# Optimization experiments

Hardware: AMD Instinct MI355X
Metric: run time of the kernel (lower is better)

The kernel has to match this reference:

```python
import jax, jax.numpy as jnp
import numpy as np

EPS = 1e-08

def setup_inputs() -> dict:
    key = jax.random.key(0)
    k1, k2 = jax.random.split(key)
    h = jax.random.normal(k1, (4, 4096, 2048), dtype=jnp.float32)
    vectors = jax.random.normal(k2, (16, 2048), dtype=jnp.float32) * 0.01
    return {"h": h, "vectors": vectors}

def reference(h, vectors):
    # Chain of k Householder reflections applied sequentially (loop-carried h).
    def step(h, v):
        v_norm_sq = jnp.maximum(jnp.dot(v, v), EPS)
        proj = jnp.einsum('bsd,d->bs', h, v)  # [B,S]
        h = h - (2.0 / v_norm_sq) * proj[..., None] * v
        return h, None
    h, _ = jax.lax.scan(step, h, vectors)
    return h
```

## Files before the change

kernel.cpp:

```cpp
#include <hip/hip_runtime.h>

#define HH_EPS 1e-8f

constexpr int D      = 2048;
constexpr int K      = 16;
constexpr int R      = 4;
constexpr int CHUNKS = D / (64 * 4);
constexpr int NROWS  = 4 * 4096;

__global__ void __launch_bounds__(64) hh_norms_kernel(const float* __restrict__ vecs,
                                                      float* __restrict__ c) {
    int k = blockIdx.x;
    int lane = threadIdx.x;
    const float4* v4 = (const float4*)(vecs + k * D);
    float s = 0.f;
#pragma unroll
    for (int j = 0; j < CHUNKS; ++j) {
        float4 v = v4[j * 64 + lane];
        s += v.x * v.x + v.y * v.y + v.z * v.z + v.w * v.w;
    }
#pragma unroll
    for (int off = 32; off >= 1; off >>= 1)
        s += __shfl_xor(s, off);
    if (lane == 0) c[k] = 2.0f / fmaxf(s, HH_EPS);
}

__device__ __forceinline__ void hh_phase(float4 (&h)[R][CHUNKS],
                                         float4 (&vcur)[CHUNKS],
                                         float4 (&vnext)[CHUNKS],
                                         const float4* __restrict__ v4base,
                                         const float* __restrict__ c,
                                         int k, int lane) {
    const float4* vn = v4base + ((k + 1) & 15) * (D / 4);
#pragma unroll
    for (int j = 0; j < CHUNKS; ++j)
        vnext[j] = vn[j * 64 + lane];

    float ck = c[k];

    float dot[R];
#pragma unroll
    for (int r = 0; r < R; ++r) dot[r] = 0.f;
#pragma unroll
    for (int j = 0; j < CHUNKS; ++j) {
#pragma unroll
        for (int r = 0; r < R; ++r) {
            dot[r] += h[r][j].x * vcur[j].x + h[r][j].y * vcur[j].y
                    + h[r][j].z * vcur[j].z + h[r][j].w * vcur[j].w;
        }
    }

#pragma unroll
    for (int off = 32; off >= 1; off >>= 1) {
#pragma unroll
        for (int r = 0; r < R; ++r)
            dot[r] += __shfl_xor(dot[r], off);
    }

    float t[R];
#pragma unroll
    for (int r = 0; r < R; ++r) t[r] = ck * dot[r];

#pragma unroll
    for (int j = 0; j < CHUNKS; ++j) {
#pragma unroll
        for (int r = 0; r < R; ++r) {
            h[r][j].x -= t[r] * vcur[j].x;
            h[r][j].y -= t[r] * vcur[j].y;
            h[r][j].z -= t[r] * vcur[j].z;
            h[r][j].w -= t[r] * vcur[j].w;
        }
    }
}

__global__ void __launch_bounds__(256, 2) hh_apply_kernel(const float* __restrict__ h_in,
                                                          const float* __restrict__ vecs,
                                                          const float* __restrict__ c,
                                                          float* __restrict__ h_out) {
    int wave = (int)((blockIdx.x * blockDim.x + threadIdx.x) >> 6);
    int lane = threadIdx.x & 63;
    int base_row = wave * R;

    float4 h[R][CHUNKS];
#pragma unroll
    for (int r = 0; r < R; ++r) {
        const float4* row = (const float4*)(h_in + (size_t)(base_row + r) * D);
#pragma unroll
        for (int j = 0; j < CHUNKS; ++j)
            h[r][j] = row[j * 64 + lane];
    }

    const float4* v4base = (const float4*)vecs;

    float4 va[CHUNKS], vb[CHUNKS];
#pragma unroll
    for (int j = 0; j < CHUNKS; ++j)
        va[j] = v4base[j * 64 + lane];

#pragma unroll 1
    for (int k = 0; k < K; k += 2) {
        hh_phase(h, va, vb, v4base, c, k, lane);
        hh_phase(h, vb, va, v4base, c, k + 1, lane);
    }

#pragma unroll
    for (int r = 0; r < R; ++r) {
        float4* row = (float4*)(h_out + (size_t)(base_row + r) * D);
#pragma unroll
        for (int j = 0; j < CHUNKS; ++j)
            row[j * 64 + lane] = h[r][j];
    }
}

extern "C" void kernel_launch(void* const* d_in, const int* in_sizes, int n_in,
                              void* d_out, int out_size, void* d_ws, size_t ws_size,
                              hipStream_t stream) {
    const float* h    = (const float*)d_in[0];
    const float* vecs = (const float*)d_in[1];
    float* out        = (float*)d_out;
    float* c          = (float*)d_ws;

    hh_norms_kernel<<<K, 64, 0, stream>>>(vecs, c);

    int waves  = NROWS / R;
    int blocks = waves * 64 / 256;
    hh_apply_kernel<<<blocks, 256, 0, stream>>>(h, vecs, c, out);
}
```

Measured before the change: 302.3 us.

## Apply Householder chain via compact WY form with LDS-staged vectors

Replaces the 16 sequential reflect steps, each with its own cross-lane reduction, with a compact WY formulation. A Gram matrix and a triangular T factor are precomputed in two small kernels. The apply kernel then computes all 16 projections, does a single batched shuffle reduction, mixes the projections through T, and applies the rank-16 update. Vectors are staged group by group into LDS through direct global-to-LDS loads, and rows per wave drop from 4 to 2. This removes the serial per-step reductions and the dependency chain, at the cost of extra launches, block-level barriers and a slightly different floating-point ordering.

Result: slower. 1.160 ms (+283.6%).

```diff
diff --git a/kernel.cpp b/kernel.cpp
--- a/kernel.cpp
+++ b/kernel.cpp
@@ -2,114 +2,164 @@
 
 #define HH_EPS 1e-8f
 
-constexpr int D      = 2048;
-constexpr int K      = 16;
-constexpr int R      = 4;
-constexpr int CHUNKS = D / (64 * 4);
-constexpr int NROWS  = 4 * 4096;
+constexpr int D     = 2048;
+constexpr int K     = 16;
+constexpr int R     = 2;
+constexpr int CH    = D / (64 * 4);
+constexpr int NROWS = 4 * 4096;
+constexpr int GV    = 4;
+constexpr int NG    = K / GV;
+constexpr int WPB   = 4;
 
-__global__ void __launch_bounds__(64) hh_norms_kernel(const float* __restrict__ vecs,
-                                                      float* __restrict__ c) {
-    int k = blockIdx.x;
+__global__ void __launch_bounds__(64) hh_gram_kernel(const float* __restrict__ vecs,
+                                                     float* __restrict__ G) {
+    int i = blockIdx.x >> 4, j = blockIdx.x & 15;
     int lane = threadIdx.x;
-    const float4* v4 = (const float4*)(vecs + k * D);
+    const float4* a = (const float4*)(vecs + i * D);
+    const float4* b = (const float4*)(vecs + j * D);
     float s = 0.f;
 #pragma unroll
-    for (int j = 0; j < CHUNKS; ++j) {
-        float4 v = v4[j * 64 + lane];
-        s += v.x * v.x + v.y * v.y + v.z * v.z + v.w * v.w;
+    for (int c = 0; c < CH; ++c) {
+        float4 x = a[c * 64 + lane], y = b[c * 64 + lane];
+        s += x.x * y.x + x.y * y.y + x.z * y.z + x.w * y.w;
     }
 #pragma unroll
-    for (int off = 32; off >= 1; off >>= 1)
-        s += __shfl_xor(s, off);
-    if (lane == 0) c[k] = 2.0f / fmaxf(s, HH_EPS);
+    for (int off = 32; off >= 1; off >>= 1) s += __shfl_xor(s, off);
+    if (lane == 0) G[i * K + j] = s;
 }
 
-__device__ __forceinline__ void hh_phase(float4 (&h)[R][CHUNKS],
-                                         float4 (&vcur)[CHUNKS],
-                                         float4 (&vnext)[CHUNKS],
-                                         const float4* __restrict__ v4base,
-                                         const float* __restrict__ c,
-                                         int k, int lane) {
-    const float4* vn = v4base + ((k + 1) & 15) * (D / 4);
+__global__ void __launch_bounds__(256) hh_buildT_kernel(const float* __restrict__ G,
+                                                        float* __restrict__ T) {
+    __shared__ float sG[K * K], sT[K * K];
+    int t = threadIdx.x;
+    if (t < K * K) { sG[t] = G[t]; sT[t] = 0.f; }
+    __syncthreads();
+    for (int k = 0; k < K; ++k) {
+        float beta = 2.f / fmaxf(sG[k * K + k], HH_EPS);
+        if (t == k) sT[k * K + k] = beta;
+        else if (t < k) {
+            float s = 0.f;
+            for (int j = t; j < k; ++j) s += sT[t * K + j] * sG[j * K + k];
+            sT[t * K + k] = -beta * s;
+        }
+        __syncthreads();
+    }
+    if (t < K * K) T[t] = sT[t];
+}
+
+__device__ __forceinline__ void stage_group(const float4* __restrict__ vsrc,
+                                            float4* svp, int g, int t) {
+    const float4* src = vsrc + g * (GV * D / 4);
 #pragma unroll
-    for (int j = 0; j < CHUNKS; ++j)
-        vnext[j] = vn[j * 64 + lane];
+    for (int i = 0; i < (GV * D / 4) / 256; ++i) {
+        int idx = t + i * 256;
+        __builtin_amdgcn_global_load_lds(
+            (const __attribute__((address_space(1))) unsigned int*)(src + idx),
+            (__attribute__((address_space(3))) unsigned int*)(svp + idx),
+            16, 0, 0);
+    }
+}
 
-    float ck = c[k];
+__global__ void __launch_bounds__(256, 3)
+hh_apply_wy(const float* __restrict__ h_in, const float* __restrict__ vecs,
+            const float* __restrict__ Tmat, float* __restrict__ h_out) {
+    __shared__ float4 sv[GV * (D / 4)];
+    __shared__ float  sT[K * K];
 
-    float dot[R];
+    const int t    = threadIdx.x;
+    const int wave = t >> 6;
+    const int lane = t & 63;
+    const int gw   = blockIdx.x * WPB + wave;
+    const size_t rbase = (size_t)gw * R;
+
+    float4 h[R][CH];
+    const float4* hin4 = (const float4*)h_in;
 #pragma unroll
-    for (int r = 0; r < R; ++r) dot[r] = 0.f;
+    for (int r = 0; r < R; ++r)
 #pragma unroll
-    for (int j = 0; j < CHUNKS; ++j) {
+        for (int j = 0; j < CH; ++j)
+            h[r][j] = hin4[(rbase + r) * (D / 4) + j * 64 + lane];
+
+    if (t < K * K) sT[t] = Tmat[t];
+
+    const float4* v4 = (const float4*)vecs;
+    stage_group(v4, sv, 0, t);
+    __syncthreads();
+
+    float P[R][K];
 #pragma unroll
-        for (int r = 0; r < R; ++r) {
-            dot[r] += h[r][j].x * vcur[j].x + h[r][j].y * vcur[j].y
-                    + h[r][j].z * vcur[j].z + h[r][j].w * vcur[j].w;
+    for (int g = 0; g < NG; ++g) {
+#pragma unroll
+        for (int lv = 0; lv < GV; ++lv) {
+            const int k = g * GV + lv;
+            float4 a0 = {0.f, 0.f, 0.f, 0.f}, a1 = {0.f, 0.f, 0.f, 0.f};
+#pragma unroll
+            for (int j = 0; j < CH; ++j) {
+                float4 v = sv[lv * (D / 4) + j * 64 + lane];
+                a0.x += h[0][j].x * v.x; a0.y += h[0][j].y * v.y;
+                a0.z += h[0][j].z * v.z; a0.w += h[0][j].w * v.w;
+                a1.x += h[1][j].x * v.x; a1.y += h[1][j].y * v.y;
+                a1.z += h[1][j].z * v.z; a1.w += h[1][j].w * v.w;
+            }
+            P[0][k] = (a0.x + a0.y) + (a0.z + a0.w);
+            P[1][k] = (a1.x + a1.y) + (a1.z + a1.w);
+        }
+        if (g < NG - 1) {
+            __syncthreads();
+            stage_group(v4, sv, g + 1, t);
+            __syncthreads();
         }
     }
 
 #pragma unroll
-    for (int off = 32; off >= 1; off >>= 1) {
+    for (int off = 32; off >= 1; off >>= 1)
 #pragma unroll
         for (int r = 0; r < R; ++r)
-            dot[r] += __shfl_xor(dot[r], off);
-    }
-
-    float t[R];
 #pragma unroll
-    for (int r = 0; r < R; ++r) t[r] = ck * dot[r];
+            for (int k = 0; k < K; ++k)
+                P[r][k] += __shfl_xor(P[r][k], off);
 
 #pragma unroll
-    for (int j = 0; j < CHUNKS; ++j) {
+    for (int j = K - 1; j >= 0; --j) {
+        float s0 = 0.f, s1 = 0.f;
 #pragma unroll
-        for (int r = 0; r < R; ++r) {
-            h[r][j].x -= t[r] * vcur[j].x;
-            h[r][j].y -= t[r] * vcur[j].y;
-            h[r][j].z -= t[r] * vcur[j].z;
-            h[r][j].w -= t[r] * vcur[j].w;
+        for (int k = 0; k <= j; ++k) {
+            float tk = sT[k * K + j];
+            s0 += P[0][k] * tk;
+            s1 += P[1][k] * tk;
         }
-    }
-}
-
-__global__ void __launch_bounds__(256, 2) hh_apply_kernel(const float* __restrict__ h_in,
-                                                          const float* __restrict__ vecs,
-                                                          const float* __restrict__ c,
-                                                          float* __restrict__ h_out) {
-    int wave = (int)((blockIdx.x * blockDim.x + threadIdx.x) >> 6);
-    int lane = threadIdx.x & 63;
-    int base_row = wave * R;
-
-    float4 h[R][CHUNKS];
-#pragma unroll
-    for (int r = 0; r < R; ++r) {
-        const float4* row = (const float4*)(h_in + (size_t)(base_row + r) * D);
-#pragma unroll
-        for (int j = 0; j < CHUNKS; ++j)
-            h[r][j] = row[j * 64 + lane];
-    }
-
-    const float4* v4base = (const float4*)vecs;
-
-    float4 va[CHUNKS], vb[CHUNKS];
-#pragma unroll
-    for (int j = 0; j < CHUNKS; ++j)
-        va[j] = v4base[j * 64 + lane];
-
-#pragma unroll 1
-    for (int k = 0; k < K; k += 2) {
-        hh_phase(h, va, vb, v4base, c, k, lane);
-        hh_phase(h, vb, va, v4base, c, k + 1, lane);
+        P[0][j] = s0; P[1][j] = s1;
     }
 
 #pragma unroll
-    for (int r = 0; r < R; ++r) {
-        float4* row = (float4*)(h_out + (size_t)(base_row + r) * D);
+    for (int gg = 0; gg < NG; ++gg) {
+        const int g = NG - 1 - gg;
 #pragma unroll
-        for (int j = 0; j < CHUNKS; ++j)
-            row[j * 64 + lane] = h[r][j];
+        for (int lv = 0; lv < GV; ++lv) {
+            const int k = g * GV + lv;
+            const float w0 = P[0][k], w1 = P[1][k];
+#pragma unroll
+            for (int j = 0; j < CH; ++j) {
+                float4 v = sv[lv * (D / 4) + j * 64 + lane];
+                h[0][j].x -= w0 * v.x; h[0][j].y -= w0 * v.y;
+                h[0][j].z -= w0 * v.z; h[0][j].w -= w0 * v.w;
+                h[1][j].x -= w1 * v.x; h[1][j].y -= w1 * v.y;
+                h[1][j].z -= w1 * v.z; h[1][j].w -= w1 * v.w;
+            }
+        }
+        if (g > 0) {
+            __syncthreads();
+            stage_group(v4, sv, g - 1, t);
+            __syncthreads();
+        }
     }
+
+    float4* out4 = (float4*)h_out;
+#pragma unroll
+    for (int r = 0; r < R; ++r)
+#pragma unroll
+        for (int j = 0; j < CH; ++j)
+            out4[(rbase + r) * (D / 4) + j * 64 + lane] = h[r][j];
 }
 
 extern "C" void kernel_launch(void* const* d_in, const int* in_sizes, int n_in,
@@ -118,11 +168,13 @@
     const float* h    = (const float*)d_in[0];
     const float* vecs = (const float*)d_in[1];
     float* out        = (float*)d_out;
-    float* c          = (float*)d_ws;
 
-    hh_norms_kernel<<<K, 64, 0, stream>>>(vecs, c);
+    float* G  = (float*)d_ws;
+    float* Tm = G + K * K;
 
-    int waves  = NROWS / R;
-    int blocks = waves * 64 / 256;
-    hh_apply_kernel<<<blocks, 256, 0, stream>>>(h, vecs, c, out);
+    hh_gram_kernel<<<K * K, 64, 0, stream>>>(vecs, G);
+    hh_buildT_kernel<<<1, 256, 0, stream>>>(G, Tm);
+
+    int blocks = NROWS / (R * WPB);
+    hh_apply_wy<<<blocks, 256, 0, stream>>>(h, vecs, Tm, out);
 }
```
